# Kernel tuning notes

Measured on AMD Instinct MI355X. Metric: run time of the kernel, lower is better.

The kernel has to match this reference:

```python
import jax, jax.numpy as jnp
import numpy as np

LONG, LAT, T, B, H, NL = 64, 64, 12, 1024, 256, 2
N = LONG * LAT        # 4096 grid nodes
D = 16 * 16           # 256, lin1_size**2


def _build_adj():
    # Faithful reconstruction of GNNLayer's sparse COO adjacency (duplicates sum,
    # as torch sparse matmul does): identity + symmetric 8-neighbor stencil for
    # interior indices i in [lat+1, (long-1)*lat-1). Each undirected edge is
    # inserted twice (once from each endpoint's loop), so interior weights are 2.
    A = np.zeros((N, N), np.float32)
    A[np.arange(N), np.arange(N)] = 1.0
    i = np.arange(LAT + 1, (LONG - 1) * LAT - 1)
    offs = np.array([-1, 1, LAT, -LAT, LAT - 1, LAT + 1, -LAT - 1, -LAT + 1])
    rows = np.repeat(i, 8)
    cols = (i[:, None] + offs).ravel()
    np.add.at(A, (rows, cols), 1.0)
    np.add.at(A, (cols, rows), 1.0)
    return jnp.asarray(A)


def setup_inputs() -> dict:
    key = jax.random.key(0)
    ks = jax.random.split(key, 12)
    s = lambda k, shape, fan: (jax.random.normal(k, shape, jnp.float32) / np.sqrt(fan)).astype(jnp.float32)
    return {
        "x":  jax.random.normal(ks[0], (T, B, LONG, LAT), jnp.float32),
        "h0": jax.random.normal(ks[1], (NL, B, H), jnp.float32),
        "A":  _build_adj(),
        "W_gnn": s(ks[2], (D, N), N), "b_gnn": jnp.zeros((D,), jnp.float32),
        "W_lin": s(ks[3], (D, D), D), "b_lin": jnp.zeros((D,), jnp.float32),
        "Wih0": s(ks[4], (3 * H, D), D), "Whh0": s(ks[5], (3 * H, H), H),
        "bih0": jnp.zeros((3 * H,), jnp.float32), "bhh0": jnp.zeros((3 * H,), jnp.float32),
        "Wih1": s(ks[6], (3 * H, H), H), "Whh1": s(ks[7], (3 * H, H), H),
        "bih1": jnp.zeros((3 * H,), jnp.float32), "bhh1": jnp.zeros((3 * H,), jnp.float32),
        "Wf0": s(ks[8], (16, H), H), "bf0": jnp.zeros((16,), jnp.float32),
        "Wf1": s(ks[9], (16, 16), 16), "bf1": jnp.zeros((16,), jnp.float32),
        "Wf2": s(ks[10], (1, 16), 16), "bf2": jnp.zeros((1,), jnp.float32),
    }


def _gru_layer(xs, h0, Wih, Whh, bih, bhh):
    # xs: [T, B, In]; PyTorch GRU cell equations, input projection hoisted out of scan.
    xW = jnp.einsum('tbd,hd->tbh', xs, Wih) + bih  # [T, B, 3H]
    def step(h, xw):
        hW = h @ Whh.T + bhh
        ri, zi, ni = jnp.split(xw, 3, axis=-1)
        rh, zh, nh = jnp.split(hW, 3, axis=-1)
        r = jax.nn.sigmoid(ri + rh)
        z = jax.nn.sigmoid(zi + zh)
        n = jnp.tanh(ni + r * nh)
        hn = (1.0 - z) * n + z * h
        return hn, hn
    _, hs = jax.lax.scan(step, h0, xW)
    return hs  # [T, B, H]


def reference(x, h0, A, W_gnn, b_gnn, W_lin, b_lin,
              Wih0, Whh0, bih0, bhh0, Wih1, Whh1, bih1, bhh1,
              Wf0, bf0, Wf1, bf1, Wf2, bf2):
    xf = x.reshape(T, B, N)                                   # flatten grid per step
    h1 = jnp.einsum('tbn,mn->tbm', xf, A)                     # (A @ x^T)^T, all steps at once
    t2 = jax.nn.sigmoid(h1 @ W_gnn.T + b_gnn)                 # GNNLayer lin1 + sigmoid
    t4 = jax.nn.sigmoid(t2 @ W_lin.T + b_lin)                 # HailNet lin1 + sigmoid -> [T,B,256]
    hs = _gru_layer(t4, h0[0], Wih0, Whh0, bih0, bhh0)
    hs = _gru_layer(hs, h0[1], Wih1, Whh1, bih1, bhh1)
    out = hs[-1]                                              # last timestep, [B, H]
    out = jax.nn.sigmoid(out @ Wf0.T + bf0)
    out = jax.nn.sigmoid(out @ Wf1.T + bf1)
    out = jax.nn.sigmoid(out @ Wf2.T + bf2)                   # [B, 1]
    return out
```

## Files before the change

### kernel.cpp

```cpp
#include <hip/hip_runtime.h>
#include <hip/hip_bf16.h>

typedef __bf16 bf16;
typedef __bf16 bf16x4 __attribute__((ext_vector_type(4)));
typedef __bf16 bf16x8 __attribute__((ext_vector_type(8)));
typedef float  f32x4  __attribute__((ext_vector_type(4)));

__device__ __forceinline__ float sigf(float x) { return 1.f / (1.f + __expf(-x)); }
__device__ __forceinline__ float tanhf_fast(float x) { return 1.f - 2.f / (1.f + __expf(2.f * x)); }

__global__ __launch_bounds__(256) void k_weff(const float* __restrict__ A,
                                              const float* __restrict__ Wg,
                                              bf16* __restrict__ Weff) {
    int n = blockIdx.x * 256 + threadIdx.x;
    const int offs[9] = {0, -1, 1, 64, -64, 63, 65, -65, -63};
    float w[9];
    int   m[9];
#pragma unroll
    for (int j = 0; j < 9; j++) {
        int mm = n + offs[j];
        bool ok = (mm >= 0 && mm < 4096);
        m[j] = ok ? mm : 0;
        w[j] = ok ? A[(size_t)n * 4096 + mm] : 0.f;
    }
    int d0 = blockIdx.y * 64;
    for (int d = d0; d < d0 + 64; d++) {
        const float* wr = Wg + (size_t)d * 4096;
        float acc = 0.f;
#pragma unroll
        for (int j = 0; j < 9; j++) acc += w[j] * wr[m[j]];
        Weff[(size_t)d * 4096 + n] = (bf16)acc;
    }
}

__global__ __launch_bounds__(256) void k_conv(const float* __restrict__ a,
                                              bf16* __restrict__ o, int ntot) {
    int i = blockIdx.x * 256 + threadIdx.x;
    if (i < ntot) o[i] = (bf16)a[i];
}

__global__ __launch_bounds__(256) void k_packW(const float* __restrict__ W,
                                               bf16* __restrict__ out) {
    int fl = blockIdx.x * 256 + threadIdx.x;
    int lane = fl & 63;
    int kt = (fl >> 6) & 7;
    int c  = (fl >> 9) % 6;
    int wv = (fl >> 9) / 6;
    int l16 = lane & 15, q = lane >> 4;
    int g = c >> 1;
    int wr = g * 256 + wv * 32 + (c & 1) * 16 + l16;
    const float* p = W + (size_t)wr * 256 + kt * 32 + q * 8;
    float4 f0 = *(const float4*)p, f1 = *(const float4*)(p + 4);
    bf16x8 v;
    v[0] = (bf16)f0.x; v[1] = (bf16)f0.y; v[2] = (bf16)f0.z; v[3] = (bf16)f0.w;
    v[4] = (bf16)f1.x; v[5] = (bf16)f1.y; v[6] = (bf16)f1.z; v[7] = (bf16)f1.w;
    *(bf16x8*)(out + (size_t)fl * 8) = v;
}

template <int K, int NTOT, int ACT, bool AF32>
__global__ __launch_bounds__(256) void k_gemm(const void* __restrict__ Ap,
                                              const bf16* __restrict__ Bp,
                                              const float* __restrict__ bias,
                                              void* __restrict__ Cp) {
    __shared__ bf16 sA[64 * 40];
    __shared__ bf16 sB[256 * 40];
    const int tid = threadIdx.x;
    const int lane = tid & 63, wv = tid >> 6;
    const int l16 = lane & 15, q = lane >> 4;
    const int row0 = blockIdx.x * 64;
    const int col0 = blockIdx.y * 256;
    const int ar = tid >> 2, ak = (tid & 3) * 8;

    f32x4 acc[4][4] = {};
    float4 pa0, pa1;
    bf16x8 pab;
    bf16x8 pb[4];

    auto loadA = [&](int k0) {
        if (AF32) {
            const float* p = (const float*)Ap + (size_t)(row0 + ar) * K + k0 + ak;
            pa0 = *(const float4*)p;
            pa1 = *(const float4*)(p + 4);
        } else {
            const bf16* p = (const bf16*)Ap + (size_t)(row0 + ar) * K + k0 + ak;
            pab = *(const bf16x8*)p;
        }
    };
    auto loadB = [&](int k0) {
#pragma unroll
        for (int i = 0; i < 4; i++) {
            int idx = tid + i * 256;
            int r = idx >> 2, kk = (idx & 3) * 8;
            pb[i] = *(const bf16x8*)(Bp + (size_t)(col0 + r) * K + k0 + kk);
        }
    };
    auto stage = [&]() {
        if (AF32) {
            bf16x8 v;
            v[0] = (bf16)pa0.x; v[1] = (bf16)pa0.y; v[2] = (bf16)pa0.z; v[3] = (bf16)pa0.w;
            v[4] = (bf16)pa1.x; v[5] = (bf16)pa1.y; v[6] = (bf16)pa1.z; v[7] = (bf16)pa1.w;
            *(bf16x8*)(sA + ar * 40 + ak) = v;
        } else {
            *(bf16x8*)(sA + ar * 40 + ak) = pab;
        }
#pragma unroll
        for (int i = 0; i < 4; i++) {
            int idx = tid + i * 256;
            int r = idx >> 2, kk = (idx & 3) * 8;
            *(bf16x8*)(sB + r * 40 + kk) = pb[i];
        }
    };

    loadA(0);
    loadB(0);
    const int S = K / 32;
    for (int s = 0; s < S; s++) {
        stage();
        __syncthreads();
        if (s + 1 < S) { loadA((s + 1) * 32); loadB((s + 1) * 32); }
        bf16x8 af[4], bfr[4];
#pragma unroll
        for (int tm = 0; tm < 4; tm++)
            af[tm] = *(bf16x8*)(sA + (tm * 16 + l16) * 40 + q * 8);
#pragma unroll
        for (int tn = 0; tn < 4; tn++)
            bfr[tn] = *(bf16x8*)(sB + (wv * 64 + tn * 16 + l16) * 40 + q * 8);
#pragma unroll
        for (int tm = 0; tm < 4; tm++)
#pragma unroll
            for (int tn = 0; tn < 4; tn++)
                acc[tm][tn] = __builtin_amdgcn_mfma_f32_16x16x32_bf16(
                    af[tm], bfr[tn], acc[tm][tn], 0, 0, 0);
        __syncthreads();
    }

#pragma unroll
    for (int tm = 0; tm < 4; tm++)
#pragma unroll
        for (int tn = 0; tn < 4; tn++)
#pragma unroll
            for (int r = 0; r < 4; r++) {
                int row = row0 + tm * 16 + q * 4 + r;
                int col = col0 + wv * 64 + tn * 16 + l16;
                float v = acc[tm][tn][r] + bias[col];
                if (ACT == 1)
                    ((bf16*)Cp)[(size_t)row * NTOT + col] = (bf16)sigf(v);
                else
                    ((float*)Cp)[(size_t)row * NTOT + col] = v;
            }
}

template <int K, int CHUNK>
__global__ __launch_bounds__(256) void k_gemm_sk(const float* __restrict__ Ap,
                                                 const bf16* __restrict__ Bp,
                                                 float* __restrict__ Cpart) {
    __shared__ bf16 sA[64 * 40];
    __shared__ bf16 sB[256 * 40];
    const int tid = threadIdx.x;
    const int lane = tid & 63, wv = tid >> 6;
    const int l16 = lane & 15, q = lane >> 4;
    const int row0 = blockIdx.x * 64;
    const int kb = blockIdx.y * CHUNK;
    float* Cp = Cpart + (size_t)blockIdx.y * 12288 * 256;
    const int ar = tid >> 2, ak = (tid & 3) * 8;

    f32x4 acc[4][4] = {};
    float4 pa0, pa1;
    bf16x8 pb[4];

    auto loadA = [&](int k0) {
        const float* p = Ap + (size_t)(row0 + ar) * K + kb + k0 + ak;
        pa0 = *(const float4*)p;
        pa1 = *(const float4*)(p + 4);
    };
    auto loadB = [&](int k0) {
#pragma unroll
        for (int i = 0; i < 4; i++) {
            int idx = tid + i * 256;
            int r = idx >> 2, kk = (idx & 3) * 8;
            pb[i] = *(const bf16x8*)(Bp + (size_t)r * K + kb + k0 + kk);
        }
    };
    auto stage = [&]() {
        bf16x8 v;
        v[0] = (bf16)pa0.x; v[1] = (bf16)pa0.y; v[2] = (bf16)pa0.z; v[3] = (bf16)pa0.w;
        v[4] = (bf16)pa1.x; v[5] = (bf16)pa1.y; v[6] = (bf16)pa1.z; v[7] = (bf16)pa1.w;
        *(bf16x8*)(sA + ar * 40 + ak) = v;
#pragma unroll
        for (int i = 0; i < 4; i++) {
            int idx = tid + i * 256;
            int r = idx >> 2, kk = (idx & 3) * 8;
            *(bf16x8*)(sB + r * 40 + kk) = pb[i];
        }
    };

    loadA(0);
    loadB(0);
    const int S = CHUNK / 32;
    for (int s = 0; s < S; s++) {
        stage();
        __syncthreads();
        if (s + 1 < S) { loadA((s + 1) * 32); loadB((s + 1) * 32); }
        bf16x8 af[4], bfr[4];
#pragma unroll
        for (int tm = 0; tm < 4; tm++)
            af[tm] = *(bf16x8*)(sA + (tm * 16 + l16) * 40 + q * 8);
#pragma unroll
        for (int tn = 0; tn < 4; tn++)
            bfr[tn] = *(bf16x8*)(sB + (wv * 64 + tn * 16 + l16) * 40 + q * 8);
#pragma unroll
        for (int tm = 0; tm < 4; tm++)
#pragma unroll
            for (int tn = 0; tn < 4; tn++)
                acc[tm][tn] = __builtin_amdgcn_mfma_f32_16x16x32_bf16(
                    af[tm], bfr[tn], acc[tm][tn], 0, 0, 0);
        __syncthreads();
    }

#pragma unroll
    for (int tm = 0; tm < 4; tm++)
#pragma unroll
        for (int tn = 0; tn < 4; tn++)
#pragma unroll
            for (int r = 0; r < 4; r++) {
                int row = row0 + tm * 16 + q * 4 + r;
                int col = wv * 64 + tn * 16 + l16;
                Cp[(size_t)row * 256 + col] = acc[tm][tn][r];
            }
}

__global__ __launch_bounds__(256) void k_reduce(const float* __restrict__ Cpart,
                                                const float* __restrict__ bias,
                                                bf16* __restrict__ t2) {
    const size_t STRIDE = (size_t)12288 * 256;
    size_t i = ((size_t)blockIdx.x * 256 + threadIdx.x) * 4;
    f32x4 s = *(const f32x4*)(Cpart + i);
#pragma unroll
    for (int ks = 1; ks < 4; ks++) {
        f32x4 p = *(const f32x4*)(Cpart + ks * STRIDE + i);
        s[0] += p[0]; s[1] += p[1]; s[2] += p[2]; s[3] += p[3];
    }
    int col = (int)(i & 255);
    const float4 b = *(const float4*)(bias + col);
    bf16x4 o;
    o[0] = (bf16)sigf(s[0] + b.x);
    o[1] = (bf16)sigf(s[1] + b.y);
    o[2] = (bf16)sigf(s[2] + b.z);
    o[3] = (bf16)sigf(s[3] + b.w);
    *(bf16x4*)(t2 + i) = o;
}

__global__ __launch_bounds__(512, 2) void k_gru(const float* __restrict__ xw,
                                                const bf16* __restrict__ Wpk,
                                                const float* __restrict__ bhh,
                                                const float* __restrict__ h0,
                                                bf16* __restrict__ hs_out,
                                                float* __restrict__ hfin) {
    __shared__ bf16 hl[16 * 264];
    const int tid = threadIdx.x, lane = tid & 63, wv = tid >> 6;
    const int l16 = lane & 15, q = lane >> 4;
    const int row0 = blockIdx.x * 16;
    const bf16* wb = Wpk + (size_t)wv * 6 * 8 * 64 * 8;

    float bh[6];
#pragma unroll
    for (int c = 0; c < 6; c++) {
        int g = c >> 1;
        bh[c] = bhh[g * 256 + wv * 32 + (c & 1) * 16 + l16];
    }
    float hreg[2][4];
#pragma unroll
    for (int hc = 0; hc < 2; hc++)
#pragma unroll
        for (int r = 0; r < 4; r++) {
            int row = q * 4 + r, col = wv * 32 + hc * 16 + l16;
            float h = h0[(size_t)(row0 + row) * 256 + col];
            hreg[hc][r] = h;
            hl[row * 264 + col] = (bf16)h;
        }
    __syncthreads();

    for (int t = 0; t < 12; t++) {
        f32x4 acc[6] = {};
        bf16x8 bc[6], bn[6];
#pragma unroll
        for (int c = 0; c < 6; c++)
            bc[c] = *(const bf16x8*)(wb + ((size_t)(c * 8 + 0) * 64 + lane) * 8);
#pragma unroll
        for (int kt = 0; kt < 8; kt++) {
            bf16x8 a = *(bf16x8*)(hl + l16 * 264 + kt * 32 + q * 8);
            if (kt < 7) {
#pragma unroll
                for (int c = 0; c < 6; c++)
                    bn[c] = *(const bf16x8*)(wb + ((size_t)(c * 8 + kt + 1) * 64 + lane) * 8);
            }
#pragma unroll
            for (int c = 0; c < 6; c++)
                acc[c] = __builtin_amdgcn_mfma_f32_16x16x32_bf16(a, bc[c], acc[c], 0, 0, 0);
#pragma unroll
            for (int c = 0; c < 6; c++) bc[c] = bn[c];
        }
        __syncthreads();
#pragma unroll
        for (int hc = 0; hc < 2; hc++)
#pragma unroll
            for (int r = 0; r < 4; r++) {
                int row = q * 4 + r, col = wv * 32 + hc * 16 + l16;
                const float* xb = xw + ((size_t)t * 1024 + row0 + row) * 768 + col;
                float rv = sigf(xb[0] + acc[hc][r] + bh[hc]);
                float zv = sigf(xb[256] + acc[2 + hc][r] + bh[2 + hc]);
                float nv = tanhf_fast(xb[512] + rv * (acc[4 + hc][r] + bh[4 + hc]));
                float hn = (1.f - zv) * nv + zv * hreg[hc][r];
                hreg[hc][r] = hn;
                bf16 hb = (bf16)hn;
                hl[row * 264 + col] = hb;
                if (hs_out) hs_out[((size_t)t * 1024 + row0 + row) * 256 + col] = hb;
            }
        __syncthreads();
    }
    if (hfin) {
#pragma unroll
        for (int hc = 0; hc < 2; hc++)
#pragma unroll
            for (int r = 0; r < 4; r++) {
                int row = q * 4 + r, col = wv * 32 + hc * 16 + l16;
                hfin[(size_t)(row0 + row) * 256 + col] = hreg[hc][r];
            }
    }
}

__global__ __launch_bounds__(256) void k_final(const float* __restrict__ h,
                                               const float* __restrict__ Wf0, const float* __restrict__ bf0,
                                               const float* __restrict__ Wf1, const float* __restrict__ bf1,
                                               const float* __restrict__ Wf2, const float* __restrict__ bf2,
                                               float* __restrict__ out) {
    __shared__ float sh[16 * 257];
    __shared__ float sy0[16 * 17];
    __shared__ float sy1[16 * 17];
    int tid = threadIdx.x;
    int r0 = blockIdx.x * 16;
#pragma unroll
    for (int i = 0; i < 16; i++) {
        int idx = tid + i * 256;
        int rr = idx >> 8, cc = idx & 255;
        sh[rr * 257 + cc] = h[(size_t)(r0 + rr) * 256 + cc];
    }
    __syncthreads();
    int rl = tid >> 4, j = tid & 15;
    float acc = bf0[j];
    for (int k = 0; k < 256; k++) acc += sh[rl * 257 + k] * Wf0[j * 256 + k];
    sy0[rl * 17 + j] = sigf(acc);
    __syncthreads();
    float acc1 = bf1[j];
#pragma unroll
    for (int k = 0; k < 16; k++) acc1 += sy0[rl * 17 + k] * Wf1[j * 16 + k];
    sy1[rl * 17 + j] = sigf(acc1);
    __syncthreads();
    if (tid < 16) {
        float a2 = bf2[0];
#pragma unroll
        for (int k = 0; k < 16; k++) a2 += sy1[tid * 17 + k] * Wf2[k];
        out[r0 + tid] = sigf(a2);
    }
}

extern "C" void kernel_launch(void* const* d_in, const int* in_sizes, int n_in,
                              void* d_out, int out_size, void* d_ws, size_t ws_size,
                              hipStream_t stream) {
    const float* x    = (const float*)d_in[0];
    const float* h0   = (const float*)d_in[1];
    const float* A    = (const float*)d_in[2];
    const float* Wgnn = (const float*)d_in[3];
    const float* bgnn = (const float*)d_in[4];
    const float* Wlin = (const float*)d_in[5];
    const float* blin = (const float*)d_in[6];
    const float* Wih0 = (const float*)d_in[7];
    const float* Whh0 = (const float*)d_in[8];
    const float* bih0 = (const float*)d_in[9];
    const float* bhh0 = (const float*)d_in[10];
    const float* Wih1 = (const float*)d_in[11];
    const float* Whh1 = (const float*)d_in[12];
    const float* bih1 = (const float*)d_in[13];
    const float* bhh1 = (const float*)d_in[14];
    const float* Wf0  = (const float*)d_in[15];
    const float* bf0  = (const float*)d_in[16];
    const float* Wf1  = (const float*)d_in[17];
    const float* bf1  = (const float*)d_in[18];
    const float* Wf2  = (const float*)d_in[19];
    const float* bf2  = (const float*)d_in[20];
    float* out = (float*)d_out;

    char* w = (char*)d_ws;
    bf16* Weff  = (bf16*)w;  w += (size_t)256 * 4096 * 2;
    bf16* WlinB = (bf16*)w;  w += (size_t)256 * 256 * 2;
    bf16* Wih0B = (bf16*)w;  w += (size_t)768 * 256 * 2;
    bf16* Wih1B = (bf16*)w;  w += (size_t)768 * 256 * 2;
    bf16* Wpk0  = (bf16*)w;  w += (size_t)768 * 256 * 2;
    bf16* Wpk1  = (bf16*)w;  w += (size_t)768 * 256 * 2;
    bf16* t2    = (bf16*)w;  w += (size_t)12288 * 256 * 2;
    bf16* t4    = (bf16*)w;  w += (size_t)12288 * 256 * 2;
    float* Cpart = (float*)w;
    float* xwb  = (float*)w;                    w += (size_t)12288 * 768 * 4;
    bf16* hs    = (bf16*)w;                     w += (size_t)12288 * 256 * 2;
    float* hfin = (float*)w;                    w += (size_t)1024 * 256 * 4;
    (void)ws_size;

    k_weff<<<dim3(16, 4), 256, 0, stream>>>(A, Wgnn, Weff);
    k_conv<<<dim3(256), 256, 0, stream>>>(Wlin, WlinB, 256 * 256);
    k_conv<<<dim3(768), 256, 0, stream>>>(Wih0, Wih0B, 768 * 256);
    k_conv<<<dim3(768), 256, 0, stream>>>(Wih1, Wih1B, 768 * 256);
    k_packW<<<dim3(96), 256, 0, stream>>>(Whh0, Wpk0);
    k_packW<<<dim3(96), 256, 0, stream>>>(Whh1, Wpk1);

    k_gemm_sk<4096, 1024><<<dim3(192, 4), 256, 0, stream>>>(x, Weff, Cpart);
    k_reduce<<<dim3(3072), 256, 0, stream>>>(Cpart, bgnn, t2);
    k_gemm<256, 256, 1, false><<<dim3(192, 1), 256, 0, stream>>>(t2, WlinB, blin, t4);
    k_gemm<256, 768, 0, false><<<dim3(192, 3), 256, 0, stream>>>(t4, Wih0B, bih0, xwb);
    k_gru<<<dim3(64), 512, 0, stream>>>(xwb, Wpk0, bhh0, h0, hs, nullptr);
    k_gemm<256, 768, 0, false><<<dim3(192, 3), 256, 0, stream>>>(hs, Wih1B, bih1, xwb);
    k_gru<<<dim3(64), 512, 0, stream>>>(xwb, Wpk1, bhh1, h0 + (size_t)1024 * 256, nullptr, hfin);
    k_final<<<dim3(64), 256, 0, stream>>>(hfin, Wf0, bf0, Wf1, bf1, Wf2, bf2, out);
}
```

Measured before the change: 663.8 us.

## Fuse both GRU layers into one recurrent kernel, dropping the layer-1 input GEMM

Replaces the two per-layer GRU launches and the intermediate layer-1 input-projection GEMM with one kernel that steps both layers together each timestep. Layer 1 computes its input projection on the fly from the fresh layer-0 hidden state in shared memory, using MFMA with packed Wih1 weights. This avoids writing and re-reading the hs sequence and the second xw buffer, and saves two launches. In exchange, each timestep does more serial work per block (three matmuls plus extra syncs) on only 64 blocks. The layer-0 xw loads are also hoisted ahead of the matmul.

Measured after the change: 997.5 us. 50.3% more time.

```diff
diff --git a/kernel.cpp b/kernel.cpp
--- a/kernel.cpp
+++ b/kernel.cpp
@@ -250,55 +250,79 @@
     *(bf16x4*)(t2 + i) = o;
 }
 
-__global__ __launch_bounds__(512, 2) void k_gru(const float* __restrict__ xw,
-                                                const bf16* __restrict__ Wpk,
-                                                const float* __restrict__ bhh,
-                                                const float* __restrict__ h0,
-                                                bf16* __restrict__ hs_out,
-                                                float* __restrict__ hfin) {
-    __shared__ bf16 hl[16 * 264];
+__global__ __launch_bounds__(512, 2) void k_gru2(const float* __restrict__ xw,
+                                                 const bf16* __restrict__ Wh0,
+                                                 const bf16* __restrict__ Wi1,
+                                                 const bf16* __restrict__ Wh1,
+                                                 const float* __restrict__ bhh0,
+                                                 const float* __restrict__ bih1,
+                                                 const float* __restrict__ bhh1,
+                                                 const float* __restrict__ h0all,
+                                                 float* __restrict__ hfin) {
+    __shared__ bf16 h0l[16 * 264];
+    __shared__ bf16 h1l[16 * 264];
     const int tid = threadIdx.x, lane = tid & 63, wv = tid >> 6;
     const int l16 = lane & 15, q = lane >> 4;
     const int row0 = blockIdx.x * 16;
-    const bf16* wb = Wpk + (size_t)wv * 6 * 8 * 64 * 8;
-
-    float bh[6];
+    const bf16* wb0 = Wh0 + (size_t)wv * 6 * 8 * 64 * 8;
+    const bf16* wbi = Wi1 + (size_t)wv * 6 * 8 * 64 * 8;
+    const bf16* wb1 = Wh1 + (size_t)wv * 6 * 8 * 64 * 8;
+
+    float bh0[6], bi1[6], bh1[6];
 #pragma unroll
     for (int c = 0; c < 6; c++) {
         int g = c >> 1;
-        bh[c] = bhh[g * 256 + wv * 32 + (c & 1) * 16 + l16];
-    }
-    float hreg[2][4];
+        int col = g * 256 + wv * 32 + (c & 1) * 16 + l16;
+        bh0[c] = bhh0[col];
+        bi1[c] = bih1[col];
+        bh1[c] = bhh1[col];
+    }
+    float h0r[2][4], h1r[2][4];
 #pragma unroll
     for (int hc = 0; hc < 2; hc++)
 #pragma unroll
         for (int r = 0; r < 4; r++) {
             int row = q * 4 + r, col = wv * 32 + hc * 16 + l16;
-            float h = h0[(size_t)(row0 + row) * 256 + col];
-            hreg[hc][r] = h;
-            hl[row * 264 + col] = (bf16)h;
+            float a = h0all[(size_t)(row0 + row) * 256 + col];
+            float b = h0all[(size_t)1024 * 256 + (size_t)(row0 + row) * 256 + col];
+            h0r[hc][r] = a; h1r[hc][r] = b;
+            h0l[row * 264 + col] = (bf16)a;
+            h1l[row * 264 + col] = (bf16)b;
         }
     __syncthreads();
 
     for (int t = 0; t < 12; t++) {
+        float xv[2][4][3];
+#pragma unroll
+        for (int hc = 0; hc < 2; hc++)
+#pragma unroll
+            for (int r = 0; r < 4; r++) {
+                const float* xb = xw + ((size_t)t * 1024 + row0 + q * 4 + r) * 768
+                                  + wv * 32 + hc * 16 + l16;
+                xv[hc][r][0] = xb[0];
+                xv[hc][r][1] = xb[256];
+                xv[hc][r][2] = xb[512];
+            }
         f32x4 acc[6] = {};
-        bf16x8 bc[6], bn[6];
-#pragma unroll
-        for (int c = 0; c < 6; c++)
-            bc[c] = *(const bf16x8*)(wb + ((size_t)(c * 8 + 0) * 64 + lane) * 8);
-#pragma unroll
-        for (int kt = 0; kt < 8; kt++) {
-            bf16x8 a = *(bf16x8*)(hl + l16 * 264 + kt * 32 + q * 8);
-            if (kt < 7) {
+        {
+            bf16x8 bc[6], bn[6];
+#pragma unroll
+            for (int c = 0; c < 6; c++)
+                bc[c] = *(const bf16x8*)(wb0 + ((size_t)(c * 8 + 0) * 64 + lane) * 8);
+#pragma unroll
+            for (int kt = 0; kt < 8; kt++) {
+                bf16x8 a = *(bf16x8*)(h0l + l16 * 264 + kt * 32 + q * 8);
+                if (kt < 7) {
+#pragma unroll
+                    for (int c = 0; c < 6; c++)
+                        bn[c] = *(const bf16x8*)(wb0 + ((size_t)(c * 8 + kt + 1) * 64 + lane) * 8);
+                }
 #pragma unroll
                 for (int c = 0; c < 6; c++)
-                    bn[c] = *(const bf16x8*)(wb + ((size_t)(c * 8 + kt + 1) * 64 + lane) * 8);
-            }
-#pragma unroll
-            for (int c = 0; c < 6; c++)
-                acc[c] = __builtin_amdgcn_mfma_f32_16x16x32_bf16(a, bc[c], acc[c], 0, 0, 0);
-#pragma unroll
-            for (int c = 0; c < 6; c++) bc[c] = bn[c];
+                    acc[c] = __builtin_amdgcn_mfma_f32_16x16x32_bf16(a, bc[c], acc[c], 0, 0, 0);
+#pragma unroll
+                for (int c = 0; c < 6; c++) bc[c] = bn[c];
+            }
         }
         __syncthreads();
 #pragma unroll
@@ -306,27 +330,72 @@
 #pragma unroll
             for (int r = 0; r < 4; r++) {
                 int row = q * 4 + r, col = wv * 32 + hc * 16 + l16;
-                const float* xb = xw + ((size_t)t * 1024 + row0 + row) * 768 + col;
-                float rv = sigf(xb[0] + acc[hc][r] + bh[hc]);
-                float zv = sigf(xb[256] + acc[2 + hc][r] + bh[2 + hc]);
-                float nv = tanhf_fast(xb[512] + rv * (acc[4 + hc][r] + bh[4 + hc]));
-                float hn = (1.f - zv) * nv + zv * hreg[hc][r];
-                hreg[hc][r] = hn;
-                bf16 hb = (bf16)hn;
-                hl[row * 264 + col] = hb;
-                if (hs_out) hs_out[((size_t)t * 1024 + row0 + row) * 256 + col] = hb;
-            }
-        __syncthreads();
-    }
-    if (hfin) {
+                float rv = sigf(xv[hc][r][0] + acc[hc][r] + bh0[hc]);
+                float zv = sigf(xv[hc][r][1] + acc[2 + hc][r] + bh0[2 + hc]);
+                float nv = tanhf_fast(xv[hc][r][2] + rv * (acc[4 + hc][r] + bh0[4 + hc]));
+                float hn = (1.f - zv) * nv + zv * h0r[hc][r];
+                h0r[hc][r] = hn;
+                h0l[row * 264 + col] = (bf16)hn;
+            }
+        __syncthreads();
+        f32x4 arz[4] = {};
+        f32x4 apn[2] = {};
+        f32x4 ahn[2] = {};
+        {
+            bf16x8 ic[6], inx[6], hcf[6], hnx[6];
+#pragma unroll
+            for (int c = 0; c < 6; c++) {
+                ic[c]  = *(const bf16x8*)(wbi + ((size_t)(c * 8 + 0) * 64 + lane) * 8);
+                hcf[c] = *(const bf16x8*)(wb1 + ((size_t)(c * 8 + 0) * 64 + lane) * 8);
+            }
+#pragma unroll
+            for (int kt = 0; kt < 8; kt++) {
+                bf16x8 a0 = *(bf16x8*)(h0l + l16 * 264 + kt * 32 + q * 8);
+                bf16x8 a1 = *(bf16x8*)(h1l + l16 * 264 + kt * 32 + q * 8);
+                if (kt < 7) {
+#pragma unroll
+                    for (int c = 0; c < 6; c++) {
+                        inx[c] = *(const bf16x8*)(wbi + ((size_t)(c * 8 + kt + 1) * 64 + lane) * 8);
+                        hnx[c] = *(const bf16x8*)(wb1 + ((size_t)(c * 8 + kt + 1) * 64 + lane) * 8);
+                    }
+                }
+#pragma unroll
+                for (int c = 0; c < 4; c++) {
+                    arz[c] = __builtin_amdgcn_mfma_f32_16x16x32_bf16(a0, ic[c], arz[c], 0, 0, 0);
+                    arz[c] = __builtin_amdgcn_mfma_f32_16x16x32_bf16(a1, hcf[c], arz[c], 0, 0, 0);
+                }
+#pragma unroll
+                for (int hc = 0; hc < 2; hc++) {
+                    apn[hc] = __builtin_amdgcn_mfma_f32_16x16x32_bf16(a0, ic[4 + hc], apn[hc], 0, 0, 0);
+                    ahn[hc] = __builtin_amdgcn_mfma_f32_16x16x32_bf16(a1, hcf[4 + hc], ahn[hc], 0, 0, 0);
+                }
+#pragma unroll
+                for (int c = 0; c < 6; c++) { ic[c] = inx[c]; hcf[c] = hnx[c]; }
+            }
+        }
+        __syncthreads();
 #pragma unroll
         for (int hc = 0; hc < 2; hc++)
 #pragma unroll
             for (int r = 0; r < 4; r++) {
                 int row = q * 4 + r, col = wv * 32 + hc * 16 + l16;
-                hfin[(size_t)(row0 + row) * 256 + col] = hreg[hc][r];
-            }
-    }
+                float rv = sigf(arz[hc][r] + bi1[hc] + bh1[hc]);
+                float zv = sigf(arz[2 + hc][r] + bi1[2 + hc] + bh1[2 + hc]);
+                float nv = tanhf_fast(apn[hc][r] + bi1[4 + hc]
+                                      + rv * (ahn[hc][r] + bh1[4 + hc]));
+                float hn = (1.f - zv) * nv + zv * h1r[hc][r];
+                h1r[hc][r] = hn;
+                if (t < 11) h1l[row * 264 + col] = (bf16)hn;
+            }
+        __syncthreads();
+    }
+#pragma unroll
+    for (int hc = 0; hc < 2; hc++)
+#pragma unroll
+        for (int r = 0; r < 4; r++) {
+            int row = q * 4 + r, col = wv * 32 + hc * 16 + l16;
+            hfin[(size_t)(row0 + row) * 256 + col] = h1r[hc][r];
+        }
 }
 
 __global__ __launch_bounds__(256) void k_final(const float* __restrict__ h,
@@ -394,30 +463,29 @@
     bf16* Weff  = (bf16*)w;  w += (size_t)256 * 4096 * 2;
     bf16* WlinB = (bf16*)w;  w += (size_t)256 * 256 * 2;
     bf16* Wih0B = (bf16*)w;  w += (size_t)768 * 256 * 2;
-    bf16* Wih1B = (bf16*)w;  w += (size_t)768 * 256 * 2;
     bf16* Wpk0  = (bf16*)w;  w += (size_t)768 * 256 * 2;
     bf16* Wpk1  = (bf16*)w;  w += (size_t)768 * 256 * 2;
+    bf16* Wpki1 = (bf16*)w;  w += (size_t)768 * 256 * 2;
     bf16* t2    = (bf16*)w;  w += (size_t)12288 * 256 * 2;
     bf16* t4    = (bf16*)w;  w += (size_t)12288 * 256 * 2;
     float* Cpart = (float*)w;
-    float* xwb  = (float*)w;                    w += (size_t)12288 * 768 * 4;
-    bf16* hs    = (bf16*)w;                     w += (size_t)12288 * 256 * 2;
-    float* hfin = (float*)w;                    w += (size_t)1024 * 256 * 4;
+    float* xwb  = (float*)w;
+    float* hfin = (float*)(w + (size_t)12288 * 768 * 4);
+    w += (size_t)4 * 12288 * 256 * 4;
     (void)ws_size;
 
     k_weff<<<dim3(16, 4), 256, 0, stream>>>(A, Wgnn, Weff);
     k_conv<<<dim3(256), 256, 0, stream>>>(Wlin, WlinB, 256 * 256);
     k_conv<<<dim3(768), 256, 0, stream>>>(Wih0, Wih0B, 768 * 256);
-    k_conv<<<dim3(768), 256, 0, stream>>>(Wih1, Wih1B, 768 * 256);
     k_packW<<<dim3(96), 256, 0, stream>>>(Whh0, Wpk0);
     k_packW<<<dim3(96), 256, 0, stream>>>(Whh1, Wpk1);
+    k_packW<<<dim3(96), 256, 0, stream>>>(Wih1, Wpki1);
 
     k_gemm_sk<4096, 1024><<<dim3(192, 4), 256, 0, stream>>>(x, Weff, Cpart);
     k_reduce<<<dim3(3072), 256, 0, stream>>>(Cpart, bgnn, t2);
     k_gemm<256, 256, 1, false><<<dim3(192, 1), 256, 0, stream>>>(t2, WlinB, blin, t4);
     k_gemm<256, 768, 0, false><<<dim3(192, 3), 256, 0, stream>>>(t4, Wih0B, bih0, xwb);
-    k_gru<<<dim3(64), 512, 0, stream>>>(xwb, Wpk0, bhh0, h0, hs, nullptr);
-    k_gemm<256, 768, 0, false><<<dim3(192, 3), 256, 0, stream>>>(hs, Wih1B, bih1, xwb);
-    k_gru<<<dim3(64), 512, 0, stream>>>(xwb, Wpk1, bhh1, h0 + (size_t)1024 * 256, nullptr, hfin);
+    k_gru2<<<dim3(64), 512, 0, stream>>>(xwb, Wpk0, Wpki1, Wpk1,
+                                         bhh0, bih1, bhh1, h0, hfin);
     k_final<<<dim3(64), 256, 0, stream>>>(hfin, Wf0, bf0, Wf1, bf1, Wf2, bf2, out);
 }
```
